# Performance work log

Hardware: AMD Instinct MI355X
Metric: run time of the kernel (lower is better)

## Reference

```python
import jax, jax.numpy as jnp
import numpy as np

B, N, E, D, H, O = 4, 10000, 160000, 128, 4, 64
NEG_SLOPE = 0.2  # PyG GATConv default


def setup_inputs() -> dict:
    key = jax.random.key(0)
    ks = jax.random.split(key, 9)
    x = jax.random.normal(ks[0], (B, N, D), jnp.float32)
    edge_index = jax.random.randint(ks[1], (2, E), 0, N, dtype=jnp.int64)
    edge_attr = jax.random.uniform(ks[2], (E,), jnp.float32)
    W_src = jax.random.normal(ks[3], (D, H, O), jnp.float32) * (1.0 / np.sqrt(D))
    att_src = jax.random.normal(ks[4], (H, O), jnp.float32) * 0.1
    att_dst = jax.random.normal(ks[5], (H, O), jnp.float32) * 0.1
    W_edge = jax.random.normal(ks[6], (H, O), jnp.float32) * 0.1  # lin_edge weight for edge_dim=1
    att_edge = jax.random.normal(ks[7], (H, O), jnp.float32) * 0.1
    bias = jnp.zeros((O,), jnp.float32)
    return {"x": x, "edge_index": edge_index, "edge_attr": edge_attr,
            "W_src": W_src, "att_src": att_src, "att_dst": att_dst,
            "W_edge": W_edge, "att_edge": att_edge, "bias": bias}


def reference(x, edge_index, edge_attr, W_src, att_src, att_dst, W_edge, att_edge, bias):
    src, dst = edge_index[0], edge_index[1]
    # shared linear projection (PyG non-bipartite GATConv): [B,N,H,O]
    h = jnp.einsum('bnd,dho->bnho', x, W_src)
    a_src = jnp.einsum('bnho,ho->bnh', h, att_src)  # [B,N,H]
    a_dst = jnp.einsum('bnho,ho->bnh', h, att_dst)  # [B,N,H]
    # edge feature projection (edge_dim=1): [E,H]
    a_edge = edge_attr[:, None] * jnp.einsum('ho,ho->h', W_edge, att_edge)[None, :]
    # attention logits per edge: [B,E,H]
    alpha = a_src[:, src] + a_dst[:, dst] + a_edge[None]
    alpha = jax.nn.leaky_relu(alpha, NEG_SLOPE)
    # segment softmax over destination nodes; segment ops need axis 0 = E
    alpha_t = jnp.transpose(alpha, (1, 0, 2))  # [E,B,H]
    m = jax.ops.segment_max(alpha_t, dst, num_segments=N)  # [N,B,H]
    m = jnp.where(jnp.isfinite(m), m, 0.0)
    p = jnp.exp(alpha_t - m[dst])
    s = jax.ops.segment_sum(p, dst, num_segments=N)
    w = p / jnp.maximum(s[dst], jnp.asarray(1e-16, p.dtype))  # [E,B,H]
    # weighted messages from source nodes, scatter-add into destinations
    msg = w[..., None] * jnp.transpose(h[:, src], (1, 0, 2, 3))  # [E,B,H,O]
    out = jax.ops.segment_sum(msg, dst, num_segments=N)  # [N,B,H,O]
    out = out.mean(axis=2) + bias  # concat=False -> mean over heads, [N,B,O]
    return jnp.transpose(out, (1, 0, 2))  # [B,N,O]
```

## Files before the change

kernel.cpp:

```cpp
#include <hip/hip_runtime.h>
#include <hip/hip_fp16.h>
#include <math.h>

constexpr int B_  = 4;
constexpr int N_  = 10000;
constexpr int E_  = 160000;
constexpr int D_  = 128;
constexpr int H_  = 4;
constexpr int O_  = 64;
constexpr float NEG_SLOPE = 0.2f;
constexpr int CAP = 64;

using half8   = __attribute__((ext_vector_type(8))) _Float16;
using f32x4   = __attribute__((ext_vector_type(4))) float;
using ushort8v = __attribute__((ext_vector_type(8))) unsigned short;

static __device__ __forceinline__ unsigned short f2h(float f) {
    return __half_as_ushort(__float2half(f));
}
static __device__ __forceinline__ float h2f(unsigned short u) {
    return __half2float(__ushort_as_half(u));
}

__global__ __launch_bounds__(256) void k_prep(
    const float* __restrict__ Wsrc, const float* __restrict__ att_src,
    const float* __restrict__ att_dst,
    const float* __restrict__ W_edge, const float* __restrict__ att_edge,
    unsigned short* __restrict__ W1t, unsigned short* __restrict__ Vt,
    int* __restrict__ deg, float* __restrict__ c)
{
    const int d = blockIdx.x;
    const int t = threadIdx.x;
    const int h = t >> 6;

    for (int i = d * 256 + t; i < N_; i += 128 * 256) deg[i] = 0;

    const float wv = Wsrc[(size_t)d * 256 + t];
    const int cc = ((t & 63) << 2) | h;
    W1t[(size_t)cc * 128 + d] = f2h(wv);

    float vs = wv * att_src[t];
    float vd = wv * att_dst[t];
#pragma unroll
    for (int off = 32; off > 0; off >>= 1) {
        vs += __shfl_down(vs, off, 64);
        vd += __shfl_down(vd, off, 64);
    }
    if ((t & 63) == 0) {
        Vt[h * 128 + d]       = f2h(vs);
        Vt[(4 + h) * 128 + d] = f2h(vd);
    }
    if (d == 1) {
#pragma unroll
        for (int k = 0; k < 4; ++k) Vt[1024 + k * 256 + t] = 0;
    }

    if (d == 0) {
        float v = W_edge[t] * att_edge[t];
#pragma unroll
        for (int off = 32; off > 0; off >>= 1) v += __shfl_down(v, off, 64);
        if ((t & 63) == 0) c[h] = v;
    }
}

__global__ __launch_bounds__(256) void k_gemm(
    const float* __restrict__ x, const int* __restrict__ ei,
    const float* __restrict__ eattr,
    const unsigned short* __restrict__ W1t, const unsigned short* __restrict__ Vt,
    unsigned short* __restrict__ hbw, float* __restrict__ asrc, float* __restrict__ adst,
    int* __restrict__ deg, int2* __restrict__ srcea)
{
    constexpr int ROWS = 32;
    constexpr int APAD = 136;
    __shared__ uint4 SHq[1024];
    unsigned short* A1 = (unsigned short*)SHq;
    unsigned short* Cb = (unsigned short*)SHq;

    const int t = threadIdx.x;
    const int w = t >> 6;
    const int lane = t & 63;
    const int i = lane & 15;
    const int q = lane >> 4;
    const size_t rowbase = (size_t)blockIdx.x * ROWS;

    int e_src = 0, e_dst = 0; float e_ea = 0.f;
    if (t < 128) {
        const int ee = blockIdx.x * 128 + t;
        e_dst = ei[E_ + ee];
        e_src = ei[ee];
        e_ea  = eattr[ee];
    }

    half8 breg[4][4];
#pragma unroll
    for (int ks = 0; ks < 4; ++ks)
#pragma unroll
        for (int ctl = 0; ctl < 4; ++ctl) {
            const size_t boff = (size_t)((w * 4 + ctl) * 16 + i) * 128 + ks * 32 + q * 8;
            breg[ks][ctl] = *(const half8*)&W1t[boff];
        }
    half8 vreg[4];
    if (w < 2) {
#pragma unroll
        for (int ks = 0; ks < 4; ++ks)
            vreg[ks] = *(const half8*)&Vt[i * 128 + ks * 32 + q * 8];
    }

    {
        const float4* xg = (const float4*)(x + rowbase * D_);
#pragma unroll
        for (int it = 0; it < 4; ++it) {
            const int idx = it * 256 + t;
            const int row = idx >> 5;
            const int c4  = idx & 31;
            float4 xv = xg[idx];
            ushort4 h1;
            h1.x = f2h(xv.x); h1.y = f2h(xv.y);
            h1.z = f2h(xv.z); h1.w = f2h(xv.w);
            *(ushort4*)&A1[row * APAD + c4 * 4] = h1;
        }
    }
    __syncthreads();

    if (t < 128) {
        const int r = atomicAdd(&deg[e_dst], 1);
        srcea[e_dst * CAP + r] = make_int2(e_src, __float_as_int(e_ea));
    }

    f32x4 acc[2][4];
#pragma unroll
    for (int tl = 0; tl < 2; ++tl)
#pragma unroll
        for (int ctl = 0; ctl < 4; ++ctl) acc[tl][ctl] = (f32x4){0.f, 0.f, 0.f, 0.f};
    f32x4 accV = (f32x4){0.f, 0.f, 0.f, 0.f};

#pragma unroll
    for (int ks = 0; ks < 4; ++ks) {
        const int a0off = i * APAD + ks * 32 + q * 8;
        const int a1off = (16 + i) * APAD + ks * 32 + q * 8;
        half8 at0 = *(const half8*)&A1[a0off];
        half8 at1 = *(const half8*)&A1[a1off];
#pragma unroll
        for (int ctl = 0; ctl < 4; ++ctl) {
            acc[0][ctl] = __builtin_amdgcn_mfma_f32_16x16x32_f16(at0, breg[ks][ctl], acc[0][ctl], 0, 0, 0);
            acc[1][ctl] = __builtin_amdgcn_mfma_f32_16x16x32_f16(at1, breg[ks][ctl], acc[1][ctl], 0, 0, 0);
        }
        if (w < 2) {
            const half8 atV = (w == 0) ? at0 : at1;
            accV = __builtin_amdgcn_mfma_f32_16x16x32_f16(atV, vreg[ks], accV, 0, 0, 0);
        }
    }

    if (w < 2 && i < 8) {
#pragma unroll
        for (int r = 0; r < 4; ++r) {
            const int row = w * 16 + q * 4 + r;
            const size_t rg = rowbase + row;
            if (i < 4) asrc[rg * 4 + i]       = accV[r];
            else       adst[rg * 4 + (i - 4)] = accV[r];
        }
    }

    __syncthreads();
#pragma unroll
    for (int tl = 0; tl < 2; ++tl) {
#pragma unroll
        for (int ctl = 0; ctl < 4; ++ctl) {
            const int col = (w * 4 + ctl) * 16 + i;
            const int chnk = col >> 3;
            const int within = col & 7;
#pragma unroll
            for (int r = 0; r < 4; ++r) {
                const int row = tl * 16 + q * 4 + r;
                const int s = chnk ^ row;
                Cb[row * 256 + s * 8 + within] = f2h(acc[tl][ctl][r]);
            }
        }
    }
    __syncthreads();
    {
        const int chnk = t & 31;
#pragma unroll
        for (int k = 0; k < 4; ++k) {
            const int row = k * 8 + (t >> 5);
            const int s = chnk ^ row;
            const uint4 v = *(const uint4*)&Cb[row * 256 + s * 8];
            *(uint4*)&hbw[(rowbase + row) * 256 + chnk * 8] = v;
        }
    }
}

__global__ __launch_bounds__(256) void k_agg(
    const int* __restrict__ deg, const int2* __restrict__ srcea,
    const float* __restrict__ asrc, const float* __restrict__ adst,
    const float* __restrict__ cvec, const unsigned short* __restrict__ hbu,
    const float* __restrict__ bias, float* __restrict__ out)
{
    __shared__ float pS[4][64][4];
    __shared__ int   baseS[4][64];

    const int b    = blockIdx.x & 3;
    const int g    = blockIdx.x >> 2;
    const int wave = threadIdx.x >> 6;
    const int lane = threadIdx.x & 63;
    const int dst  = g * 4 + wave;

    const int dg    = deg[dst];
    const int ebase = dst * CAP;

    const float4 ad = *(const float4*)&adst[((size_t)b * N_ + dst) * 4];
    const float4 cc = *(const float4*)cvec;

    const int half = lane >> 5;
    const int ol   = (lane & 31) * 8;

    float acc[4][2][4];
#pragma unroll
    for (int u = 0; u < 4; ++u)
#pragma unroll
        for (int oo = 0; oo < 2; ++oo)
#pragma unroll
            for (int h = 0; h < 4; ++h) acc[u][oo][h] = 0.f;
    float q0 = 0.f, q1 = 0.f, q2 = 0.f, q3 = 0.f;

    for (int c0 = 0; c0 < dg; c0 += 64) {
        const int jl = c0 + lane;
        const bool valid = jl < dg;
        const int2 rec = srcea[ebase + (valid ? jl : 0)];
        const int   srcl = rec.x;
        const float ea   = __int_as_float(rec.y);
        const float4 as = *(const float4*)&asrc[((size_t)b * N_ + srcl) * 4];
        float4 al;
        al.x = as.x + ad.x + ea * cc.x;
        al.y = as.y + ad.y + ea * cc.y;
        al.z = as.z + ad.z + ea * cc.z;
        al.w = as.w + ad.w + ea * cc.w;
        al.x = al.x > 0.f ? al.x : NEG_SLOPE * al.x;
        al.y = al.y > 0.f ? al.y : NEG_SLOPE * al.y;
        al.z = al.z > 0.f ? al.z : NEG_SLOPE * al.z;
        al.w = al.w > 0.f ? al.w : NEG_SLOPE * al.w;
        const float px = valid ? __expf(al.x) : 0.f;
        const float py = valid ? __expf(al.y) : 0.f;
        const float pz = valid ? __expf(al.z) : 0.f;
        const float pw = valid ? __expf(al.w) : 0.f;
        q0 += px; q1 += py; q2 += pz; q3 += pw;

        *(float4*)&pS[wave][lane][0] = make_float4(px, py, pz, pw);
        baseS[wave][lane] = (b * N_ + srcl) << 8;
        __builtin_amdgcn_wave_barrier();

        const int cnt = min(64, dg - c0);
        for (int j = 0; j < cnt; j += 8) {
#pragma unroll
            for (int u = 0; u < 4; ++u) {
                const int idx = j + 2 * u + half;
                const float4 p = *(const float4*)&pS[wave][idx][0];
                const int    r = baseS[wave][idx];
                const ushort8v hh = *(const ushort8v*)&hbu[(size_t)r + ol];
                acc[u][0][0] = fmaf(p.x, h2f(hh[0]), acc[u][0][0]);
                acc[u][0][1] = fmaf(p.y, h2f(hh[1]), acc[u][0][1]);
                acc[u][0][2] = fmaf(p.z, h2f(hh[2]), acc[u][0][2]);
                acc[u][0][3] = fmaf(p.w, h2f(hh[3]), acc[u][0][3]);
                acc[u][1][0] = fmaf(p.x, h2f(hh[4]), acc[u][1][0]);
                acc[u][1][1] = fmaf(p.y, h2f(hh[5]), acc[u][1][1]);
                acc[u][1][2] = fmaf(p.z, h2f(hh[6]), acc[u][1][2]);
                acc[u][1][3] = fmaf(p.w, h2f(hh[7]), acc[u][1][3]);
            }
        }
        __builtin_amdgcn_wave_barrier();
    }

    float tt[2][4];
#pragma unroll
    for (int oo = 0; oo < 2; ++oo)
#pragma unroll
        for (int h = 0; h < 4; ++h)
            tt[oo][h] = (acc[0][oo][h] + acc[1][oo][h]) + (acc[2][oo][h] + acc[3][oo][h]);

#pragma unroll
    for (int oo = 0; oo < 2; ++oo)
#pragma unroll
        for (int h = 0; h < 4; ++h)
            tt[oo][h] += __shfl_xor(tt[oo][h], 32, 64);

#pragma unroll
    for (int off = 32; off > 0; off >>= 1) {
        q0 += __shfl_xor(q0, off, 64);
        q1 += __shfl_xor(q1, off, 64);
        q2 += __shfl_xor(q2, off, 64);
        q3 += __shfl_xor(q3, off, 64);
    }

    if (lane < 32) {
        const float i0 = 1.f / fmaxf(q0, 1e-16f);
        const float i1 = 1.f / fmaxf(q1, 1e-16f);
        const float i2 = 1.f / fmaxf(q2, 1e-16f);
        const float i3 = 1.f / fmaxf(q3, 1e-16f);
        const float2 bs = *(const float2*)&bias[lane * 2];
        float2 res;
        res.x = 0.25f * (tt[0][0] * i0 + tt[0][1] * i1 + tt[0][2] * i2 + tt[0][3] * i3) + bs.x;
        res.y = 0.25f * (tt[1][0] * i0 + tt[1][1] * i1 + tt[1][2] * i2 + tt[1][3] * i3) + bs.y;
        *(float2*)&out[((size_t)b * N_ + dst) * O_ + lane * 2] = res;
    }
}

extern "C" void kernel_launch(void* const* d_in, const int* in_sizes, int n_in,
                              void* d_out, int out_size, void* d_ws, size_t ws_size,
                              hipStream_t stream)
{
    (void)in_sizes; (void)n_in; (void)out_size; (void)ws_size;
    const float* x        = (const float*)d_in[0];
    const int*   ei       = (const int*)d_in[1];
    const float* eattr    = (const float*)d_in[2];
    const float* Wsrc     = (const float*)d_in[3];
    const float* att_src  = (const float*)d_in[4];
    const float* att_dst  = (const float*)d_in[5];
    const float* W_edge   = (const float*)d_in[6];
    const float* att_edge = (const float*)d_in[7];
    const float* bias     = (const float*)d_in[8];
    float* out = (float*)d_out;

    char* w = (char*)d_ws;
    auto take = [&](size_t bytes) { char* p = w; w += (bytes + 15) & ~size_t(15); return p; };
    unsigned short* hb   = (unsigned short*)take((size_t)B_ * N_ * O_ * H_ * 2);
    float* asrc    = (float*)take((size_t)B_ * N_ * H_ * 4);
    float* adst    = (float*)take((size_t)B_ * N_ * H_ * 4);
    float* c       = (float*)take(4 * 4);
    unsigned short* W1t = (unsigned short*)take((size_t)256 * 128 * 2);
    unsigned short* Vt  = (unsigned short*)take((size_t)16 * 128 * 2);
    int* deg       = (int*)take((size_t)N_ * 4);
    int2* srcea    = (int2*)take((size_t)N_ * CAP * 8);

    hipLaunchKernelGGL(k_prep, dim3(128), dim3(256), 0, stream,
                       Wsrc, att_src, att_dst, W_edge, att_edge,
                       W1t, Vt, deg, c);
    hipLaunchKernelGGL(k_gemm, dim3((B_ * N_) / 32), dim3(256), 0, stream,
                       x, ei, eattr, W1t, Vt, hb, asrc, adst, deg, srcea);
    hipLaunchKernelGGL(k_agg, dim3(N_ / 4 * B_), dim3(256), 0, stream,
                       deg, srcea, asrc, adst, c, hb, bias, out);
}
```

Before: 161.0 us.

## Normalize attention before aggregation with fdot2, split edge placement into separate blocks

The aggregation kernel now computes the softmax over all of a node's edges in one pass, assuming degree never exceeds 64. It folds the normalization into fp16 per-edge weights and accumulates messages with packed fp16 dot2 instructions across heads, which cuts the accumulator registers from 32 to 8. Edge bucketing (the atomic degree count and srcea write) moves out of the GEMM blocks into extra dedicated blocks of the same launch. The risks are lower precision from fp16 weights and truncation if any node has more than 64 incoming edges.

```diff
diff --git a/kernel.cpp b/kernel.cpp
--- a/kernel.cpp
+++ b/kernel.cpp
@@ -10,8 +10,11 @@
 constexpr int O_  = 64;
 constexpr float NEG_SLOPE = 0.2f;
 constexpr int CAP = 64;
+constexpr int GEMM_BLOCKS  = (B_ * N_) / 32;
+constexpr int PLACE_BLOCKS = E_ / 256;
 
 using half8   = __attribute__((ext_vector_type(8))) _Float16;
+using half2v  = __attribute__((ext_vector_type(2))) _Float16;
 using f32x4   = __attribute__((ext_vector_type(4))) float;
 using ushort8v = __attribute__((ext_vector_type(8))) unsigned short;
 
@@ -21,6 +24,14 @@
 static __device__ __forceinline__ float h2f(unsigned short u) {
     return __half2float(__ushort_as_half(u));
 }
+
+#if __has_builtin(__builtin_amdgcn_fdot2)
+#define FDOT2(a, b, c) __builtin_amdgcn_fdot2((a), (b), (c), false)
+#else
+static __device__ __forceinline__ float FDOT2(half2v a, half2v b, float c) {
+    return c + (float)a[0] * (float)b[0] + (float)a[1] * (float)b[1];
+}
+#endif
 
 __global__ __launch_bounds__(256) void k_prep(
     const float* __restrict__ Wsrc, const float* __restrict__ att_src,
@@ -77,19 +88,20 @@
     unsigned short* Cb = (unsigned short*)SHq;
 
     const int t = threadIdx.x;
+
+    if (blockIdx.x >= GEMM_BLOCKS) {
+        const int e = (blockIdx.x - GEMM_BLOCKS) * 256 + t;
+        const int dstn = ei[E_ + e];
+        const int r = atomicAdd(&deg[dstn], 1);
+        srcea[dstn * CAP + r] = make_int2(ei[e], __float_as_int(eattr[e]));
+        return;
+    }
+
     const int w = t >> 6;
     const int lane = t & 63;
     const int i = lane & 15;
     const int q = lane >> 4;
     const size_t rowbase = (size_t)blockIdx.x * ROWS;
-
-    int e_src = 0, e_dst = 0; float e_ea = 0.f;
-    if (t < 128) {
-        const int ee = blockIdx.x * 128 + t;
-        e_dst = ei[E_ + ee];
-        e_src = ei[ee];
-        e_ea  = eattr[ee];
-    }
 
     half8 breg[4][4];
 #pragma unroll
@@ -122,11 +134,6 @@
     }
     __syncthreads();
 
-    if (t < 128) {
-        const int r = atomicAdd(&deg[e_dst], 1);
-        srcea[e_dst * CAP + r] = make_int2(e_src, __float_as_int(e_ea));
-    }
-
     f32x4 acc[2][4];
 #pragma unroll
     for (int tl = 0; tl < 2; ++tl)
@@ -196,8 +203,7 @@
     const float* __restrict__ cvec, const unsigned short* __restrict__ hbu,
     const float* __restrict__ bias, float* __restrict__ out)
 {
-    __shared__ float pS[4][64][4];
-    __shared__ int   baseS[4][64];
+    __shared__ uint4 jS[4][64];
 
     const int b    = blockIdx.x & 3;
     const int g    = blockIdx.x >> 2;
@@ -211,77 +217,25 @@
     const float4 ad = *(const float4*)&adst[((size_t)b * N_ + dst) * 4];
     const float4 cc = *(const float4*)cvec;
 
-    const int half = lane >> 5;
-    const int ol   = (lane & 31) * 8;
-
-    float acc[4][2][4];
-#pragma unroll
-    for (int u = 0; u < 4; ++u)
-#pragma unroll
-        for (int oo = 0; oo < 2; ++oo)
-#pragma unroll
-            for (int h = 0; h < 4; ++h) acc[u][oo][h] = 0.f;
-    float q0 = 0.f, q1 = 0.f, q2 = 0.f, q3 = 0.f;
-
-    for (int c0 = 0; c0 < dg; c0 += 64) {
-        const int jl = c0 + lane;
-        const bool valid = jl < dg;
-        const int2 rec = srcea[ebase + (valid ? jl : 0)];
-        const int   srcl = rec.x;
-        const float ea   = __int_as_float(rec.y);
-        const float4 as = *(const float4*)&asrc[((size_t)b * N_ + srcl) * 4];
-        float4 al;
-        al.x = as.x + ad.x + ea * cc.x;
-        al.y = as.y + ad.y + ea * cc.y;
-        al.z = as.z + ad.z + ea * cc.z;
-        al.w = as.w + ad.w + ea * cc.w;
-        al.x = al.x > 0.f ? al.x : NEG_SLOPE * al.x;
-        al.y = al.y > 0.f ? al.y : NEG_SLOPE * al.y;
-        al.z = al.z > 0.f ? al.z : NEG_SLOPE * al.z;
-        al.w = al.w > 0.f ? al.w : NEG_SLOPE * al.w;
-        const float px = valid ? __expf(al.x) : 0.f;
-        const float py = valid ? __expf(al.y) : 0.f;
-        const float pz = valid ? __expf(al.z) : 0.f;
-        const float pw = valid ? __expf(al.w) : 0.f;
-        q0 += px; q1 += py; q2 += pz; q3 += pw;
-
-        *(float4*)&pS[wave][lane][0] = make_float4(px, py, pz, pw);
-        baseS[wave][lane] = (b * N_ + srcl) << 8;
-        __builtin_amdgcn_wave_barrier();
-
-        const int cnt = min(64, dg - c0);
-        for (int j = 0; j < cnt; j += 8) {
-#pragma unroll
-            for (int u = 0; u < 4; ++u) {
-                const int idx = j + 2 * u + half;
-                const float4 p = *(const float4*)&pS[wave][idx][0];
-                const int    r = baseS[wave][idx];
-                const ushort8v hh = *(const ushort8v*)&hbu[(size_t)r + ol];
-                acc[u][0][0] = fmaf(p.x, h2f(hh[0]), acc[u][0][0]);
-                acc[u][0][1] = fmaf(p.y, h2f(hh[1]), acc[u][0][1]);
-                acc[u][0][2] = fmaf(p.z, h2f(hh[2]), acc[u][0][2]);
-                acc[u][0][3] = fmaf(p.w, h2f(hh[3]), acc[u][0][3]);
-                acc[u][1][0] = fmaf(p.x, h2f(hh[4]), acc[u][1][0]);
-                acc[u][1][1] = fmaf(p.y, h2f(hh[5]), acc[u][1][1]);
-                acc[u][1][2] = fmaf(p.z, h2f(hh[6]), acc[u][1][2]);
-                acc[u][1][3] = fmaf(p.w, h2f(hh[7]), acc[u][1][3]);
-            }
-        }
-        __builtin_amdgcn_wave_barrier();
-    }
-
-    float tt[2][4];
-#pragma unroll
-    for (int oo = 0; oo < 2; ++oo)
-#pragma unroll
-        for (int h = 0; h < 4; ++h)
-            tt[oo][h] = (acc[0][oo][h] + acc[1][oo][h]) + (acc[2][oo][h] + acc[3][oo][h]);
-
-#pragma unroll
-    for (int oo = 0; oo < 2; ++oo)
-#pragma unroll
-        for (int h = 0; h < 4; ++h)
-            tt[oo][h] += __shfl_xor(tt[oo][h], 32, 64);
+    const bool valid = lane < dg;
+    const int2 rec = srcea[ebase + (valid ? lane : 0)];
+    const int   srcl = valid ? rec.x : 0;
+    const float ea   = __int_as_float(rec.y);
+    const float4 as = *(const float4*)&asrc[((size_t)b * N_ + srcl) * 4];
+    float4 al;
+    al.x = as.x + ad.x + ea * cc.x;
+    al.y = as.y + ad.y + ea * cc.y;
+    al.z = as.z + ad.z + ea * cc.z;
+    al.w = as.w + ad.w + ea * cc.w;
+    al.x = al.x > 0.f ? al.x : NEG_SLOPE * al.x;
+    al.y = al.y > 0.f ? al.y : NEG_SLOPE * al.y;
+    al.z = al.z > 0.f ? al.z : NEG_SLOPE * al.z;
+    al.w = al.w > 0.f ? al.w : NEG_SLOPE * al.w;
+    float q0 = valid ? __expf(al.x) : 0.f;
+    float q1 = valid ? __expf(al.y) : 0.f;
+    float q2 = valid ? __expf(al.z) : 0.f;
+    float q3 = valid ? __expf(al.w) : 0.f;
+    const float px = q0, py = q1, pz = q2, pw = q3;
 
 #pragma unroll
     for (int off = 32; off > 0; off >>= 1) {
@@ -290,16 +244,49 @@
         q2 += __shfl_xor(q2, off, 64);
         q3 += __shfl_xor(q3, off, 64);
     }
+    const float i0 = 1.f / fmaxf(q0, 1e-16f);
+    const float i1 = 1.f / fmaxf(q1, 1e-16f);
+    const float i2 = 1.f / fmaxf(q2, 1e-16f);
+    const float i3 = 1.f / fmaxf(q3, 1e-16f);
+
+    union { half2v h; unsigned u; } u01, u23;
+    u01.h[0] = (_Float16)(px * i0); u01.h[1] = (_Float16)(py * i1);
+    u23.h[0] = (_Float16)(pz * i2); u23.h[1] = (_Float16)(pw * i3);
+    jS[wave][lane] = make_uint4((unsigned)((b * N_ + srcl) << 8), u01.u, u23.u, 0u);
+    __builtin_amdgcn_wave_barrier();
+
+    const int half = lane >> 5;
+    const int ol   = (lane & 31) * 8;
+
+    float a0[4] = {0.f, 0.f, 0.f, 0.f};
+    float a1[4] = {0.f, 0.f, 0.f, 0.f};
+
+    for (int j = 0; j < dg; j += 8) {
+#pragma unroll
+        for (int u = 0; u < 4; ++u) {
+            const int idx = j + 2 * u + half;
+            const uint4 e4 = jS[wave][idx];
+            const ushort8v hh = *(const ushort8v*)&hbu[(size_t)e4.x + ol];
+            union { ushort8v s; half2v h[4]; } H; H.s = hh;
+            union { unsigned u; half2v h; } p01, p23;
+            p01.u = e4.y; p23.u = e4.z;
+            a0[u] = FDOT2(H.h[0], p01.h, a0[u]);
+            a0[u] = FDOT2(H.h[1], p23.h, a0[u]);
+            a1[u] = FDOT2(H.h[2], p01.h, a1[u]);
+            a1[u] = FDOT2(H.h[3], p23.h, a1[u]);
+        }
+    }
+
+    float t0 = (a0[0] + a0[1]) + (a0[2] + a0[3]);
+    float t1 = (a1[0] + a1[1]) + (a1[2] + a1[3]);
+    t0 += __shfl_xor(t0, 32, 64);
+    t1 += __shfl_xor(t1, 32, 64);
 
     if (lane < 32) {
-        const float i0 = 1.f / fmaxf(q0, 1e-16f);
-        const float i1 = 1.f / fmaxf(q1, 1e-16f);
-        const float i2 = 1.f / fmaxf(q2, 1e-16f);
-        const float i3 = 1.f / fmaxf(q3, 1e-16f);
         const float2 bs = *(const float2*)&bias[lane * 2];
         float2 res;
-        res.x = 0.25f * (tt[0][0] * i0 + tt[0][1] * i1 + tt[0][2] * i2 + tt[0][3] * i3) + bs.x;
-        res.y = 0.25f * (tt[1][0] * i0 + tt[1][1] * i1 + tt[1][2] * i2 + tt[1][3] * i3) + bs.y;
+        res.x = 0.25f * t0 + bs.x;
+        res.y = 0.25f * t1 + bs.y;
         *(float2*)&out[((size_t)b * N_ + dst) * O_ + lane * 2] = res;
     }
 }
@@ -334,7 +321,7 @@
     hipLaunchKernelGGL(k_prep, dim3(128), dim3(256), 0, stream,
                        Wsrc, att_src, att_dst, W_edge, att_edge,
                        W1t, Vt, deg, c);
-    hipLaunchKernelGGL(k_gemm, dim3((B_ * N_) / 32), dim3(256), 0, stream,
+    hipLaunchKernelGGL(k_gemm, dim3(GEMM_BLOCKS + PLACE_BLOCKS), dim3(256), 0, stream,
                        x, ei, eattr, W1t, Vt, hb, asrc, adst, deg, srcea);
     hipLaunchKernelGGL(k_agg, dim3(N_ / 4 * B_), dim3(256), 0, stream,
                        deg, srcea, asrc, adst, c, hb, bias, out);
```

New measurement: 136.1 us. 1.18x faster.
